# Kernel optimization log

Hardware: AMD Instinct MI355X
Metric: run time of the kernel (lower is better)

Reference implementation:

```python
import jax, jax.numpy as jnp
import numpy as np

# dims: T tokens, HID hidden, H heads, D head_dim, K conv kernel size
T, HID, H, D, K = 4096, 2048, 16, 128, 4
HD = H * D
EPS = 1e-6


def causal_conv(x, w):
    # depthwise causal conv: x [T, C], w [C, K]; y_t = sum_i w[:, i] * x_{t-K+1+i}
    xp = jnp.pad(x, ((K - 1, 0), (0, 0)))
    y = jnp.zeros_like(x)
    for i in range(K):  # small fixed kernel loop
        y = y + w[:, i] * xp[i:i + x.shape[0]]
    return y


def l2norm(x):
    return x * jax.lax.rsqrt(jnp.sum(x * x, -1, keepdims=True) + EPS)


def setup_inputs() -> dict:
    key = jax.random.key(0)
    ks = jax.random.split(key, 16)
    s = lambda n: 1.0 / np.sqrt(n)
    return {
        "hidden_states": jax.random.normal(ks[0], (T, HID), jnp.float32),
        "Wq": jax.random.normal(ks[1], (HID, HD), jnp.float32) * s(HID),
        "Wk": jax.random.normal(ks[2], (HID, HD), jnp.float32) * s(HID),
        "Wv": jax.random.normal(ks[3], (HID, HD), jnp.float32) * s(HID),
        "wq_conv": jax.random.normal(ks[4], (HD, K), jnp.float32) * s(K),
        "wk_conv": jax.random.normal(ks[5], (HD, K), jnp.float32) * s(K),
        "wv_conv": jax.random.normal(ks[6], (HD, K), jnp.float32) * s(K),
        "A_log": jax.random.uniform(ks[7], (H,), jnp.float32, 0.0, 0.5),
        "dt_bias": jax.random.normal(ks[8], (HD,), jnp.float32) * 0.1,
        "Wfa": jax.random.normal(ks[9], (HID, D), jnp.float32) * s(HID),
        "Wfb": jax.random.normal(ks[10], (D, HD), jnp.float32) * s(D),
        "Wb": jax.random.normal(ks[11], (HID, H), jnp.float32) * s(HID),
        "Wga": jax.random.normal(ks[12], (HID, D), jnp.float32) * s(HID),
        "Wgb": jax.random.normal(ks[13], (D, HD), jnp.float32) * s(D),
        "norm_w": jnp.ones((D,), jnp.float32),
        "Wo": jax.random.normal(ks[14], (HD, HID), jnp.float32) * s(HD),
    }


def reference(hidden_states, Wq, Wk, Wv, wq_conv, wk_conv, wv_conv, A_log,
              dt_bias, Wfa, Wfb, Wb, Wga, Wgb, norm_w, Wo):
    x = hidden_states
    # projections + short causal conv + SiLU
    q = jax.nn.silu(causal_conv(x @ Wq, wq_conv)).reshape(T, H, D)
    k = jax.nn.silu(causal_conv(x @ Wk, wk_conv)).reshape(T, H, D)
    v = jax.nn.silu(causal_conv(x @ Wv, wv_conv)).reshape(T, H, D)
    # fine-grained per-channel log-decay: g = -exp(A_log) * softplus(f + dt_bias), [T,H,D]
    f = (x @ Wfa) @ Wfb + dt_bias
    g = -(jnp.exp(A_log)[None, :, None]) * jax.nn.softplus(f.reshape(T, H, D))
    beta = jax.nn.sigmoid(x @ Wb)  # [T, H]
    q = l2norm(q)
    k = l2norm(k)
    scale = D ** -0.5

    def step(S, inp):  # S: [H, Dk, Dv]
        q_t, k_t, v_t, g_t, b_t = inp
        S = S * jnp.exp(g_t)[..., None]  # diagonal per-key-channel decay
        err = v_t - jnp.einsum('hkv,hk->hv', S, k_t)  # delta-rule error
        dv = b_t[:, None] * err  # beta gate
        S = S + k_t[:, :, None] * dv[:, None, :]
        o_t = jnp.einsum('hkv,hk->hv', S, q_t) * scale
        return S, o_t

    S0 = jnp.zeros((H, D, D), jnp.float32)
    _, o = jax.lax.scan(step, S0, (q, k, v, g, beta))  # o: [T, H, D]

    # gated RMSNorm then output projection
    gate = ((x @ Wga) @ Wgb).reshape(T, H, D)
    o = o * jax.lax.rsqrt(jnp.mean(o * o, -1, keepdims=True) + EPS)
    o = o * norm_w * jax.nn.silu(gate)
    return o.reshape(T, HD) @ Wo
```

## Files before the change

### kernel.cpp

```cpp
#include <hip/hip_runtime.h>
#include <hip/hip_bf16.h>
#include <math.h>

typedef __bf16 bf16_t;
typedef __bf16 bf16x8 __attribute__((ext_vector_type(8)));
typedef float  floatx4 __attribute__((ext_vector_type(4)));
typedef float  floatx2 __attribute__((ext_vector_type(2)));
typedef unsigned uintx4 __attribute__((ext_vector_type(4)));

constexpr int T_TOK = 4096;
constexpr int HID   = 2048;
constexpr int NH    = 16;
constexpr int DH    = 128;
constexpr int CH    = 2048;
constexpr int CHUNK = 16;
constexpr int NCH   = T_TOK / CHUNK;

__global__ __launch_bounds__(256) void cast_to_bf16(const float* __restrict__ in,
                                                    bf16_t* __restrict__ out, int n) {
  int i = (blockIdx.x * 256 + threadIdx.x) * 8;
  if (i >= n) return;
  float4 a = *(const float4*)(in + i);
  float4 b = *(const float4*)(in + i + 4);
  bf16x8 o;
  o[0]=(bf16_t)a.x; o[1]=(bf16_t)a.y; o[2]=(bf16_t)a.z; o[3]=(bf16_t)a.w;
  o[4]=(bf16_t)b.x; o[5]=(bf16_t)b.y; o[6]=(bf16_t)b.z; o[7]=(bf16_t)b.w;
  *(bf16x8*)(out + i) = o;
}

__global__ __launch_bounds__(256) void transpose_cast(const float* __restrict__ in,
                                                      bf16_t* __restrict__ out, int R, int C) {
  __shared__ float tile[32][33];
  int tx = threadIdx.x & 31;
  int ty = threadIdx.x >> 5;
  int r0 = blockIdx.x * 32;
  int c0 = blockIdx.y * 32;
#pragma unroll
  for (int i = 0; i < 4; i++) {
    int r = ty + i * 8;
    float v = 0.f;
    if (r0 + r < R && c0 + tx < C) v = in[(size_t)(r0 + r) * C + (c0 + tx)];
    tile[r][tx] = v;
  }
  __syncthreads();
#pragma unroll
  for (int i = 0; i < 4; i++) {
    int cr = ty + i * 8;
    if (c0 + cr < C && r0 + tx < R)
      out[(size_t)(c0 + cr) * R + (r0 + tx)] = (bf16_t)tile[tx][cr];
  }
}

template<bool OUT_BF16>
__global__ __launch_bounds__(256) void gemm_bf16(
    const bf16_t* __restrict__ A, int lda,
    const bf16_t* __restrict__ Bt, int ldb,
    void* __restrict__ Cv, int ldc, int M, int N, int K) {
  __shared__ bf16_t sA[128][40];
  __shared__ bf16_t sB[128][40];
  const int tid  = threadIdx.x;
  const int bm0  = blockIdx.x * 128;
  const int bn0  = blockIdx.y * 128;
  const int wave = tid >> 6;
  const int lane = tid & 63;
  const int wm   = (wave & 1) * 64;
  const int wn   = (wave >> 1) * 64;
  const int fm   = lane & 15;
  const int kq   = lane >> 4;

  floatx4 acc[4][4];
#pragma unroll
  for (int mi = 0; mi < 4; mi++)
#pragma unroll
    for (int ni = 0; ni < 4; ni++)
      acc[mi][ni] = (floatx4){0.f, 0.f, 0.f, 0.f};

  const int sr = tid >> 2;
  const int sk = (tid & 3) * 8;
  const bool bval0 = (bn0 + sr) < N;
  const bool bval1 = (bn0 + sr + 64) < N;
  const bf16_t* Ag0 = A + (size_t)(bm0 + sr) * lda + sk;
  const bf16_t* Ag1 = Ag0 + (size_t)64 * lda;
  const bf16_t* Bg0 = Bt + (size_t)(bn0 + sr) * ldb + sk;
  const bf16_t* Bg1 = Bg0 + (size_t)64 * ldb;

  for (int k0 = 0; k0 < K; k0 += 32) {
    float4 a0 = *(const float4*)(Ag0 + k0);
    float4 a1 = *(const float4*)(Ag1 + k0);
    float4 b0 = bval0 ? *(const float4*)(Bg0 + k0) : make_float4(0.f, 0.f, 0.f, 0.f);
    float4 b1 = bval1 ? *(const float4*)(Bg1 + k0) : make_float4(0.f, 0.f, 0.f, 0.f);
    __syncthreads();
    *(float4*)(&sA[sr][sk])      = a0;
    *(float4*)(&sA[sr + 64][sk]) = a1;
    *(float4*)(&sB[sr][sk])      = b0;
    *(float4*)(&sB[sr + 64][sk]) = b1;
    __syncthreads();
    bf16x8 afr[4], bfr[4];
#pragma unroll
    for (int i = 0; i < 4; i++) {
      afr[i] = *(const bf16x8*)(&sA[wm + i * 16 + fm][kq * 8]);
      bfr[i] = *(const bf16x8*)(&sB[wn + i * 16 + fm][kq * 8]);
    }
#pragma unroll
    for (int mi = 0; mi < 4; mi++)
#pragma unroll
      for (int ni = 0; ni < 4; ni++)
        acc[mi][ni] = __builtin_amdgcn_mfma_f32_16x16x32_bf16(afr[mi], bfr[ni], acc[mi][ni], 0, 0, 0);
  }

  const int rr = (lane >> 4) * 4;
#pragma unroll
  for (int mi = 0; mi < 4; mi++) {
#pragma unroll
    for (int r = 0; r < 4; r++) {
      const int row = bm0 + wm + mi * 16 + rr + r;
#pragma unroll
      for (int ni = 0; ni < 4; ni++) {
        const int col = bn0 + wn + ni * 16 + fm;
        if (col < N) {
          if constexpr (OUT_BF16)
            ((bf16_t*)Cv)[(size_t)row * ldc + col] = (bf16_t)acc[mi][ni][r];
          else
            ((float*)Cv)[(size_t)row * ldc + col] = acc[mi][ni][r];
        }
      }
    }
  }
}

__device__ __forceinline__ void gload_lds16(const bf16_t* g, bf16_t* l) {
  __builtin_amdgcn_global_load_lds(
      (const __attribute__((address_space(1))) void*)g,
      (__attribute__((address_space(3))) void*)l, 16, 0, 0);
}

template<bool OUT_BF16>
__global__ __launch_bounds__(256) void gemm_bf16_lds(
    const bf16_t* __restrict__ A, int lda,
    const bf16_t* __restrict__ Bt, int ldb,
    void* __restrict__ Cv, int ldc, int M, int N, int K) {
  __shared__ bf16_t sA[2][128][32];
  __shared__ bf16_t sB[2][128][32];
  const int tid  = threadIdx.x;
  const int bm0  = blockIdx.x * 128;
  const int bn0  = blockIdx.y * 128;
  const int wave = tid >> 6;
  const int lane = tid & 63;
  const int wm   = (wave & 1) * 64;
  const int wn   = (wave >> 1) * 64;
  const int fm   = lane & 15;
  const int kq   = lane >> 4;

  floatx4 acc[4][4];
#pragma unroll
  for (int mi = 0; mi < 4; mi++)
#pragma unroll
    for (int ni = 0; ni < 4; ni++)
      acc[mi][ni] = (floatx4){0.f, 0.f, 0.f, 0.f};

  const int sr = tid >> 2;
  const int sk = (tid & 3) * 8;
  const bf16_t* Ag0 = A + (size_t)(bm0 + sr) * lda + sk;
  const bf16_t* Ag1 = Ag0 + (size_t)64 * lda;
  const bf16_t* Bg0 = Bt + (size_t)(bn0 + sr) * ldb + sk;
  const bf16_t* Bg1 = Bg0 + (size_t)64 * ldb;

  auto stage = [&](int b, int k0) {
    gload_lds16(Ag0 + k0, &sA[b][16 * wave][0]);
    gload_lds16(Ag1 + k0, &sA[b][64 + 16 * wave][0]);
    gload_lds16(Bg0 + k0, &sB[b][16 * wave][0]);
    gload_lds16(Bg1 + k0, &sB[b][64 + 16 * wave][0]);
  };

  stage(0, 0);
  __syncthreads();
  int cur = 0;
  for (int k0 = 0; k0 < K; k0 += 32) {
    if (k0 + 32 < K) stage(cur ^ 1, k0 + 32);
    bf16x8 afr[4], bfr[4];
#pragma unroll
    for (int i = 0; i < 4; i++) {
      afr[i] = *(const bf16x8*)(&sA[cur][wm + i * 16 + fm][kq * 8]);
      bfr[i] = *(const bf16x8*)(&sB[cur][wn + i * 16 + fm][kq * 8]);
    }
#pragma unroll
    for (int mi = 0; mi < 4; mi++)
#pragma unroll
      for (int ni = 0; ni < 4; ni++)
        acc[mi][ni] = __builtin_amdgcn_mfma_f32_16x16x32_bf16(afr[mi], bfr[ni], acc[mi][ni], 0, 0, 0);
    __syncthreads();
    cur ^= 1;
  }

  const int rr = (lane >> 4) * 4;
#pragma unroll
  for (int mi = 0; mi < 4; mi++) {
#pragma unroll
    for (int r = 0; r < 4; r++) {
      const int row = bm0 + wm + mi * 16 + rr + r;
#pragma unroll
      for (int ni = 0; ni < 4; ni++) {
        const int col = bn0 + wn + ni * 16 + fm;
        if constexpr (OUT_BF16)
          ((bf16_t*)Cv)[(size_t)row * ldc + col] = (bf16_t)acc[mi][ni][r];
        else
          ((float*)Cv)[(size_t)row * ldc + col] = acc[mi][ni][r];
      }
    }
  }
}

template<bool L2NORM>
__global__ __launch_bounds__(256) void conv_silu(
    const bf16_t* __restrict__ raw, const float* __restrict__ wconv,
    bf16_t* __restrict__ out) {
  const int t   = blockIdx.x;
  const int tid = threadIdx.x;
  const int c0  = tid * 8;

  float w[8][4];
#pragma unroll
  for (int j = 0; j < 8; j++) {
    float4 t0 = *(const float4*)(wconv + (size_t)(c0 + j) * 4);
    w[j][0] = t0.x; w[j][1] = t0.y; w[j][2] = t0.z; w[j][3] = t0.w;
  }
  float a[8] = {};
#pragma unroll
  for (int i = 0; i < 4; i++) {
    int tr = t - 3 + i;
    if (tr < 0) continue;
    bf16x8 xr = *(const bf16x8*)(raw + (size_t)tr * CH + c0);
#pragma unroll
    for (int j = 0; j < 8; j++) a[j] += w[j][i] * (float)xr[j];
  }
  float s = 0.f;
#pragma unroll
  for (int j = 0; j < 8; j++) {
    a[j] = a[j] / (1.f + expf(-a[j]));
    s += a[j] * a[j];
  }
  float rs = 1.f;
  if constexpr (L2NORM) {
#pragma unroll
    for (int m = 1; m < 16; m <<= 1) s += __shfl_xor(s, m);
    rs = rsqrtf(s + 1e-6f);
  }
  bf16x8 r;
#pragma unroll
  for (int j = 0; j < 8; j++) r[j] = (bf16_t)(a[j] * rs);
  *(bf16x8*)(out + (size_t)t * CH + c0) = r;
}

__global__ __launch_bounds__(256) void gamma_beta(
    float* __restrict__ f_gam, const float* __restrict__ dt_bias,
    const float* __restrict__ A_log, float* __restrict__ beta_io) {
  const int t   = blockIdx.x;
  const int tid = threadIdx.x;
  const int c0  = tid * 8;
  const int h   = c0 >> 7;
  const float a_h = expf(A_log[h]);
  const size_t o0 = (size_t)t * CH + c0;
  float fv[8], db[8];
  { float4 f0 = *(const float4*)(f_gam + o0);   float4 f1 = *(const float4*)(f_gam + o0 + 4);
    fv[0]=f0.x; fv[1]=f0.y; fv[2]=f0.z; fv[3]=f0.w; fv[4]=f1.x; fv[5]=f1.y; fv[6]=f1.z; fv[7]=f1.w;
    float4 d0 = *(const float4*)(dt_bias + c0); float4 d1 = *(const float4*)(dt_bias + c0 + 4);
    db[0]=d0.x; db[1]=d0.y; db[2]=d0.z; db[3]=d0.w; db[4]=d1.x; db[5]=d1.y; db[6]=d1.z; db[7]=d1.w; }
  float og[8];
#pragma unroll
  for (int j = 0; j < 8; j++) {
    float f = fv[j] + db[j];
    float sp = (f > 20.f) ? f : log1pf(expf(f));
    og[j] = -a_h * sp;
  }
  *(float4*)(f_gam + o0)     = make_float4(og[0], og[1], og[2], og[3]);
  *(float4*)(f_gam + o0 + 4) = make_float4(og[4], og[5], og[6], og[7]);
  if (tid < NH) {
    float b = beta_io[(size_t)t * NH + tid];
    beta_io[(size_t)t * NH + tid] = 1.f / (1.f + expf(-b));
  }
}

template<int IMM>
__device__ __forceinline__ float swzf(float x) {
  return __builtin_bit_cast(float, __builtin_amdgcn_ds_swizzle(__builtin_bit_cast(int, x), IMM));
}
template<int CTRL>
__device__ __forceinline__ float dppadd(float x) {
  int v = __builtin_amdgcn_update_dpp(0, __builtin_bit_cast(int, x), CTRL, 0xF, 0xF, true);
  return x + __builtin_bit_cast(float, v);
}
__device__ __forceinline__ float cumsum16(float x) {
  x = dppadd<0x111>(x);
  x = dppadd<0x112>(x);
  x = dppadd<0x114>(x);
  x = dppadd<0x118>(x);
  return x;
}
__device__ __forceinline__ floatx2 bfpair(unsigned u) {
  floatx2 r;
  r[0] = __builtin_bit_cast(float, u << 16);
  r[1] = __builtin_bit_cast(float, u & 0xFFFF0000u);
  return r;
}

__global__ __launch_bounds__(64) void wy_prep(
    bf16_t* __restrict__ qn, bf16_t* __restrict__ kn,
    const float* __restrict__ gg, const float* __restrict__ beta,
    bf16_t* __restrict__ ktilT, float* __restrict__ Tm,
    bf16_t* __restrict__ MBf, float* __restrict__ ecT, float* __restrict__ e2T) {
  const int hc = blockIdx.x;
  const int h  = hc >> 8;
  const int c  = hc & 255;
  const int l  = threadIdx.x;
  const int tl = l & 15;
  const int gr = l >> 4;

  __shared__ bf16_t KldsT[128][24];
  __shared__ float  Wlds[16][17];
  __shared__ float  Mlds[16][17];
  __shared__ float  eclds[128], e2lds[128];
  __shared__ float  blds[16];

  const int kb0 = h * DH + gr * 8;
  const size_t rowoff = (size_t)(c * CHUNK + tl) * CH;

  if (gr == 0) blds[tl] = beta[(size_t)(c * CHUNK + tl) * NH + h];

  floatx4 wt = (floatx4){0.f, 0.f, 0.f, 0.f};
  floatx4 m  = (floatx4){0.f, 0.f, 0.f, 0.f};
  bf16x8 khs[4], qhs[4];
#pragma unroll
  for (int kb = 0; kb < 4; kb++) {
    const int ke = kb0 + kb * 32;
    float4 ga = *(const float4*)(gg + rowoff + ke);
    float4 gb = *(const float4*)(gg + rowoff + ke + 4);
    float cm[8] = {ga.x, ga.y, ga.z, ga.w, gb.x, gb.y, gb.z, gb.w};
    float lamh[8], lamt[8], ec[8], e2[8];
#pragma unroll
    for (int j = 0; j < 8; j++) {
      float cs   = cumsum16(cm[j]);
      float cmid = swzf<(7 << 5) | 0x10>(cs);
      lamh[j] = __expf(cs - cmid);
      lamt[j] = __expf(cmid - cs);
      ec[j]   = __expf(cmid);
      e2[j]   = swzf<(15 << 5) | 0x10>(lamh[j]);
    }
    if (tl == 0) {
#pragma unroll
      for (int j = 0; j < 8; j++) {
        eclds[kb * 32 + gr * 8 + j] = ec[j];
        e2lds[kb * 32 + gr * 8 + j] = e2[j];
      }
    }
    uint4 kr = *(const uint4*)(kn + rowoff + ke);
    uint4 qr = *(const uint4*)(qn + rowoff + ke);
    float kf[8], qf[8];
    { floatx2 a0 = bfpair(kr.x), a1 = bfpair(kr.y), a2 = bfpair(kr.z), a3 = bfpair(kr.w);
      kf[0]=a0[0];kf[1]=a0[1];kf[2]=a1[0];kf[3]=a1[1];kf[4]=a2[0];kf[5]=a2[1];kf[6]=a3[0];kf[7]=a3[1];
      floatx2 b0 = bfpair(qr.x), b1 = bfpair(qr.y), b2 = bfpair(qr.z), b3 = bfpair(qr.w);
      qf[0]=b0[0];qf[1]=b0[1];qf[2]=b1[0];qf[3]=b1[1];qf[4]=b2[0];qf[5]=b2[1];qf[6]=b3[0];qf[7]=b3[1]; }
    bf16x8 khat, ktil, qhat;
#pragma unroll
    for (int j = 0; j < 8; j++) {
      khat[j] = (bf16_t)(kf[j] * lamh[j]);
      ktil[j] = (bf16_t)(kf[j] * lamt[j]);
      qhat[j] = (bf16_t)(qf[j] * lamh[j]);
      khs[kb][j] = (bf16_t)(kf[j] * lamh[j] * ec[j]);
      qhs[kb][j] = (bf16_t)(qf[j] * lamh[j] * ec[j]);
    }
    wt = __builtin_amdgcn_mfma_f32_16x16x32_bf16(ktil, khat, wt, 0, 0, 0);
    m  = __builtin_amdgcn_mfma_f32_16x16x32_bf16(qhat, ktil, m,  0, 0, 0);
#pragma unroll
    for (int j = 0; j < 8; j++) KldsT[kb * 32 + gr * 8 + j][tl] = ktil[j];
  }
#pragma unroll
  for (int kb = 0; kb < 4; kb++) {
    *(uint4*)(kn + rowoff + kb0 + kb * 32) = __builtin_bit_cast(uint4, khs[kb]);
    *(uint4*)(qn + rowoff + kb0 + kb * 32) = __builtin_bit_cast(uint4, qhs[kb]);
  }
#pragma unroll
  for (int ri = 0; ri < 4; ri++) {
    Wlds[tl][4 * gr + ri] = wt[ri];
    Mlds[4 * gr + ri][tl] = (4 * gr + ri >= tl) ? m[ri] : 0.f;
  }
  {
    const int j = tl;
    float x[16];
#pragma unroll
    for (int t = 0; t < 16; t++) {
      float a = 0.f;
#pragma unroll
      for (int s = 0; s < 16; s++)
        if (s < t) a = fmaf(Wlds[t][s], x[s], a);
      x[t] = (t == j) ? 1.f : ((t > j) ? -blds[t] * a : 0.f);
    }
    if (gr == 0) {
      const float bj = blds[j];
#pragma unroll
      for (int t = 0; t < 16; t++)
        Tm[((size_t)hc * 16 + t) * 16 + j] = x[t] * bj;
    }
  }
  {
    uint4 mbo = {0, 0, 0, 0};
    if (gr < 2) {
      bf16x8 mm;
#pragma unroll
      for (int jj = 0; jj < 8; jj++) mm[jj] = (bf16_t)Mlds[tl][gr * 8 + jj];
      mbo = __builtin_bit_cast(uint4, mm);
    }
    ((uint4*)MBf)[(size_t)hc * 64 + l] = mbo;
  }
  for (int i = l; i < 128; i += 64) {
    uint4 a0 = *(const uint4*)&KldsT[i][0];
    uint4 a1 = *(const uint4*)&KldsT[i][8];
    bf16_t* dst = ktilT + ((size_t)hc * 128 + i) * 16;
    *(uint4*)dst = a0;
    *(uint4*)(dst + 8) = a1;
  }
  for (int i = l; i < 128; i += 64) {
    ecT[(size_t)hc * 128 + (i & 15) * 8 + (i >> 4)] = eclds[i];
    e2T[(size_t)hc * 128 + (i & 15) * 8 + (i >> 4)] = e2lds[i];
  }
}

__global__ __launch_bounds__(128, 1) void scan_wy3(
    const bf16_t* __restrict__ khsG, const bf16_t* __restrict__ qhsG,
    const bf16_t* __restrict__ vn, const bf16_t* __restrict__ ktilT,
    const float* __restrict__ Tm, const bf16_t* __restrict__ MBf,
    const float* __restrict__ ecT, const float* __restrict__ e2T,
    float* __restrict__ o) {
  const int h   = blockIdx.x >> 3;
  const int vt  = blockIdx.x & 7;
  const int tid = threadIdx.x;
  const int wid = tid >> 6;
  const int l   = tid & 63;
  const int tl  = l & 15;
  const int gr  = l >> 4;

  __shared__ uint4   sKQ[2][8][64];
  __shared__ floatx4 sT[2][4][64];
  __shared__ uint4   sMB[2][64];
  __shared__ uint4   sKT[2][8][64];
  __shared__ floatx4 sEC[2][4][64];
  __shared__ uint2   sV[2][64];
  __shared__ float4  sO[2][64];
  __shared__ float   SldsT[16][132];
  __shared__ float   DVlds[16][17];

  const int kb0 = h * DH + gr * 8;
  const int vb0 = h * DH + vt * 16 + gr * 4;
  const size_t hcBase = (size_t)h * NCH;
  constexpr float scale = 0.08838834764831845f;

  auto produce = [&](int c, int b) {
    const size_t rowoff = (size_t)(c * CHUNK + tl) * CH;
    const size_t hc = hcBase + c;
    uint4 kq[8];
#pragma unroll
    for (int kb = 0; kb < 4; kb++) {
      kq[kb]     = *(const uint4*)(khsG + rowoff + kb0 + kb * 32);
      kq[4 + kb] = *(const uint4*)(qhsG + rowoff + kb0 + kb * 32);
    }
    const float* Trp = Tm + (hc * 16 + tl) * 16;
    floatx4 Tv[4];
#pragma unroll
    for (int j = 0; j < 4; j++) Tv[j] = *(const floatx4*)(Trp + 4 * j);
    uint4 mbv = ((const uint4*)MBf)[hc * 64 + l];
    const int g2 = gr & 1;
    uint4 ktv[8];
#pragma unroll
    for (int kt = 0; kt < 8; kt++)
      ktv[kt] = *(const uint4*)(ktilT + (hc * 128 + kt * 16 + tl) * 16 + g2 * 8);
    floatx4 ecv[4];
    ecv[0] = *(const floatx4*)(ecT + hc * 128 + tl * 8);
    ecv[1] = *(const floatx4*)(ecT + hc * 128 + tl * 8 + 4);
    ecv[2] = *(const floatx4*)(e2T + hc * 128 + tl * 8);
    ecv[3] = *(const floatx4*)(e2T + hc * 128 + tl * 8 + 4);
    uint2 vv = *(const uint2*)(vn + rowoff + vb0);
#pragma unroll
    for (int i = 0; i < 8; i++) sKQ[b][i][l] = kq[i];
#pragma unroll
    for (int j = 0; j < 4; j++) sT[b][j][l] = Tv[j];
    sMB[b][l] = mbv;
#pragma unroll
    for (int i = 0; i < 8; i++) sKT[b][i][l] = ktv[i];
#pragma unroll
    for (int j = 0; j < 4; j++) sEC[b][j][l] = ecv[j];
    sV[b][l] = vv;
  };

  float S[8][4];
#pragma unroll
  for (int kt = 0; kt < 8; kt++)
#pragma unroll
    for (int ri = 0; ri < 4; ri++) S[kt][ri] = 0.f;

  if (wid == 1) {
    produce(0, 0);
  } else {
    for (int i = l; i < 16 * 132; i += 64) (&SldsT[0][0])[i] = 0.f;
  }
  __syncthreads();

  int cur = 0;
  for (int c = 0; c < NCH; ++c) {
    if (wid == 1) {
      if (c >= 1) {
        float4 ov = sO[cur ^ 1][l];
        const size_t rowp = (size_t)((c - 1) * CHUNK + tl) * CH;
        *(float4*)(o + rowp + vb0) = ov;
      }
      produce(c + 1 < NCH ? c + 1 : NCH - 1, cur ^ 1);
    } else {
      floatx4 p  = (floatx4){0.f, 0.f, 0.f, 0.f};
      floatx4 o1 = (floatx4){0.f, 0.f, 0.f, 0.f};
#pragma unroll
      for (int kb = 0; kb < 4; kb++) {
        float4 sa = *(const float4*)(&SldsT[tl][kb * 32 + gr * 8]);
        float4 sb = *(const float4*)(&SldsT[tl][kb * 32 + gr * 8 + 4]);
        bf16x8 s0a;
        s0a[0]=(bf16_t)sa.x; s0a[1]=(bf16_t)sa.y; s0a[2]=(bf16_t)sa.z; s0a[3]=(bf16_t)sa.w;
        s0a[4]=(bf16_t)sb.x; s0a[5]=(bf16_t)sb.y; s0a[6]=(bf16_t)sb.z; s0a[7]=(bf16_t)sb.w;
        p  = __builtin_amdgcn_mfma_f32_16x16x32_bf16(s0a, __builtin_bit_cast(bf16x8, sKQ[cur][kb][l]), p,  0, 0, 0);
        o1 = __builtin_amdgcn_mfma_f32_16x16x32_bf16(s0a, __builtin_bit_cast(bf16x8, sKQ[cur][4 + kb][l]), o1, 0, 0, 0);
      }
      float acc[4];
      { uint2 vr = sV[cur][l];
        floatx2 v01 = bfpair(vr.x), v23 = bfpair(vr.y);
        acc[0] = v01[0] - p[0]; acc[1] = v01[1] - p[1];
        acc[2] = v23[0] - p[2]; acc[3] = v23[1] - p[3]; }
      *(float4*)(&DVlds[tl][4 * gr]) = make_float4(acc[0], acc[1], acc[2], acc[3]);
      floatx4 T0 = sT[cur][0][l], T1 = sT[cur][1][l], T2 = sT[cur][2][l], T3 = sT[cur][3][l];
      float dv[4] = {0.f, 0.f, 0.f, 0.f};
#pragma unroll
      for (int s = 0; s < 16; s++) {
        const float ts = (s < 4) ? T0[s] : (s < 8) ? T1[s - 4] : (s < 12) ? T2[s - 8] : T3[s - 12];
        float4 vp = *(const float4*)(&DVlds[s][4 * gr]);
        dv[0] = fmaf(ts, vp.x, dv[0]);
        dv[1] = fmaf(ts, vp.y, dv[1]);
        dv[2] = fmaf(ts, vp.z, dv[2]);
        dv[3] = fmaf(ts, vp.w, dv[3]);
      }
#pragma unroll
      for (int ri = 0; ri < 4; ri++) DVlds[tl][4 * gr + ri] = dv[ri];
      bf16x8 dva = {};
      if (gr < 2) {
#pragma unroll
        for (int jj = 0; jj < 8; jj++) dva[jj] = (bf16_t)DVlds[gr * 8 + jj][tl];
      }
      floatx4 o2 = __builtin_amdgcn_mfma_f32_16x16x32_bf16(
          dva, __builtin_bit_cast(bf16x8, sMB[cur][l]), (floatx4){0.f, 0.f, 0.f, 0.f}, 0, 0, 0);
      sO[cur][l] = make_float4((o1[0] + o2[0]) * scale, (o1[1] + o2[1]) * scale,
                               (o1[2] + o2[2]) * scale, (o1[3] + o2[3]) * scale);
      floatx4 ec0 = sEC[cur][0][l], ec1 = sEC[cur][1][l];
      floatx4 e20 = sEC[cur][2][l], e21 = sEC[cur][3][l];
#pragma unroll
      for (int kt = 0; kt < 8; kt++) {
        const float ecK = (kt < 4) ? ec0[kt] : ec1[kt - 4];
        const float e2K = (kt < 4) ? e20[kt] : e21[kt - 4];
        floatx4 sa;
#pragma unroll
        for (int ri = 0; ri < 4; ri++) sa[ri] = ecK * S[kt][ri];
        sa = __builtin_amdgcn_mfma_f32_16x16x32_bf16(
            dva, __builtin_bit_cast(bf16x8, sKT[cur][kt][l]), sa, 0, 0, 0);
#pragma unroll
        for (int ri = 0; ri < 4; ri++) S[kt][ri] = e2K * sa[ri];
      }
#pragma unroll
      for (int kt = 0; kt < 8; kt++)
#pragma unroll
        for (int ri = 0; ri < 4; ri++)
          SldsT[4 * gr + ri][kt * 16 + tl] = S[kt][ri];
    }
    __syncthreads();
    cur ^= 1;
  }
  if (wid == 1) {
    float4 ov = sO[(NCH - 1) & 1][l];
    const size_t rowp = (size_t)((NCH - 1) * CHUNK + tl) * CH;
    *(float4*)(o + rowp + vb0) = ov;
  }
}

__global__ __launch_bounds__(256) void postprocess(
    const float* __restrict__ o, const bf16_t* __restrict__ gate,
    const float* __restrict__ norm_w, bf16_t* __restrict__ og) {
  const int t = blockIdx.x, tid = threadIdx.x;
  const int c0 = tid * 8, d0 = c0 & 127;
  const size_t o0 = (size_t)t * CH + c0;
  float ov[8], gv[8], nw[8];
  { float4 a = *(const float4*)(o + o0);    float4 b = *(const float4*)(o + o0 + 4);
    ov[0]=a.x; ov[1]=a.y; ov[2]=a.z; ov[3]=a.w; ov[4]=b.x; ov[5]=b.y; ov[6]=b.z; ov[7]=b.w;
    bf16x8 g8 = *(const bf16x8*)(gate + o0);
    for (int j = 0; j < 8; j++) gv[j] = (float)g8[j];
    float4 e = *(const float4*)(norm_w + d0); float4 f = *(const float4*)(norm_w + d0 + 4);
    nw[0]=e.x; nw[1]=e.y; nw[2]=e.z; nw[3]=e.w; nw[4]=f.x; nw[5]=f.y; nw[6]=f.z; nw[7]=f.w; }
  float ss = 0.f;
#pragma unroll
  for (int j = 0; j < 8; j++) ss += ov[j] * ov[j];
#pragma unroll
  for (int m = 1; m < 16; m <<= 1) ss += __shfl_xor(ss, m);
  const float rs = rsqrtf(ss * (1.f / 128.f) + 1e-6f);
  bf16x8 r;
#pragma unroll
  for (int j = 0; j < 8; j++) {
    float g = gv[j];
    float val = ov[j] * rs * nw[j] * (g / (1.f + expf(-g)));
    r[j] = (bf16_t)val;
  }
  *(bf16x8*)(og + o0) = r;
}

static inline void launch_gemm(const bf16_t* A, int lda, const bf16_t* Bt, int ldb,
                               void* C, int ldc, int M, int N, int K, bool obf16,
                               hipStream_t s) {
  dim3 grid(M / 128, (N + 127) / 128);
  if ((N & 127) == 0) {
    if (obf16) gemm_bf16_lds<true><<<grid, 256, 0, s>>>(A, lda, Bt, ldb, C, ldc, M, N, K);
    else       gemm_bf16_lds<false><<<grid, 256, 0, s>>>(A, lda, Bt, ldb, C, ldc, M, N, K);
  } else {
    if (obf16) gemm_bf16<true><<<grid, 256, 0, s>>>(A, lda, Bt, ldb, C, ldc, M, N, K);
    else       gemm_bf16<false><<<grid, 256, 0, s>>>(A, lda, Bt, ldb, C, ldc, M, N, K);
  }
}

extern "C" void kernel_launch(void* const* d_in, const int* in_sizes, int n_in,
                              void* d_out, int out_size, void* d_ws, size_t ws_size,
                              hipStream_t stream) {
  const float* x       = (const float*)d_in[0];
  const float* Wq      = (const float*)d_in[1];
  const float* Wk      = (const float*)d_in[2];
  const float* Wv      = (const float*)d_in[3];
  const float* wqc     = (const float*)d_in[4];
  const float* wkc     = (const float*)d_in[5];
  const float* wvc     = (const float*)d_in[6];
  const float* A_log   = (const float*)d_in[7];
  const float* dt_bias = (const float*)d_in[8];
  const float* Wfa     = (const float*)d_in[9];
  const float* Wfb     = (const float*)d_in[10];
  const float* Wb      = (const float*)d_in[11];
  const float* Wga     = (const float*)d_in[12];
  const float* Wgb     = (const float*)d_in[13];
  const float* norm_w  = (const float*)d_in[14];
  const float* Wo      = (const float*)d_in[15];

  char* w = (char*)d_ws;
  size_t off = 0;
  auto give = [&](size_t bytes) -> void* {
    size_t cur = off;
    off = (off + bytes + 255) & ~(size_t)255;
    return (void*)(w + cur);
  };
  bf16_t* Wbig = (bf16_t*)give((size_t)CH * HID * 2);
  bf16_t* WfgT = (bf16_t*)give((size_t)256 * HID * 2);
  bf16_t* WfbT = (bf16_t*)give((size_t)CH * 128 * 2);
  bf16_t* WgbT = (bf16_t*)give((size_t)CH * 128 * 2);
  bf16_t* WbT  = (bf16_t*)give((size_t)NH * HID * 2);
  bf16_t* Ax   = (bf16_t*)give((size_t)T_TOK * HID * 2);
  bf16_t* raw0 = (bf16_t*)give((size_t)T_TOK * CH * 2);
  bf16_t* qnb  = (bf16_t*)give((size_t)T_TOK * CH * 2);
  bf16_t* knb  = (bf16_t*)give((size_t)T_TOK * CH * 2);
  bf16_t* vnb  = (bf16_t*)give((size_t)T_TOK * CH * 2);
  bf16_t* f1g1 = (bf16_t*)give((size_t)T_TOK * 256 * 2);
  float*  fbuf = (float*)give((size_t)T_TOK * CH * 4);
  bf16_t* gateb= (bf16_t*)give((size_t)T_TOK * CH * 2);
  float*  betab= (float*)give((size_t)T_TOK * NH * 4);
  bf16_t* ktilT= (bf16_t*)give((size_t)NH * NCH * 128 * 16 * 2);
  float*  Tmat = (float*)give((size_t)NH * NCH * 256 * 4);
  bf16_t* MBf  = (bf16_t*)give((size_t)NH * NCH * 64 * 8 * 2);
  float*  ecTb = (float*)give((size_t)NH * NCH * 128 * 4);
  float*  e2Tb = (float*)give((size_t)NH * NCH * 128 * 4);
  float*  obuf = (float*)Ax;
  bf16_t* ogb  = qnb;

  auto tr = [&](const float* in, bf16_t* out, int R, int C) {
    transpose_cast<<<dim3((R + 31) / 32, (C + 31) / 32), 256, 0, stream>>>(in, out, R, C);
  };

  cast_to_bf16<<<dim3((T_TOK * HID) / 2048), 256, 0, stream>>>(x, Ax, T_TOK * HID);
  tr(Wfa, WfgT, HID, 128);
  tr(Wga, WfgT + (size_t)128 * HID, HID, 128);
  tr(Wfb, WfbT, 128, CH);  tr(Wgb, WgbT, 128, CH);
  tr(Wb, WbT, HID, NH);

  tr(Wq, Wbig, HID, CH);
  launch_gemm(Ax, HID, Wbig, HID, raw0, CH, T_TOK, CH, HID, true, stream);
  conv_silu<true><<<dim3(T_TOK), 256, 0, stream>>>(raw0, wqc, qnb);
  tr(Wk, Wbig, HID, CH);
  launch_gemm(Ax, HID, Wbig, HID, raw0, CH, T_TOK, CH, HID, true, stream);
  conv_silu<true><<<dim3(T_TOK), 256, 0, stream>>>(raw0, wkc, knb);
  tr(Wv, Wbig, HID, CH);
  launch_gemm(Ax, HID, Wbig, HID, raw0, CH, T_TOK, CH, HID, true, stream);
  conv_silu<false><<<dim3(T_TOK), 256, 0, stream>>>(raw0, wvc, vnb);

  launch_gemm(Ax, HID, WfgT, HID, f1g1, 256, T_TOK, 256, HID, true, stream);
  launch_gemm(Ax, HID, WbT, HID, betab, NH, T_TOK, NH, HID, false, stream);
  launch_gemm(f1g1, 256, WfbT, 128, fbuf, CH, T_TOK, CH, 128, false, stream);
  launch_gemm(f1g1 + 128, 256, WgbT, 128, gateb, CH, T_TOK, CH, 128, true, stream);
  gamma_beta<<<dim3(T_TOK), 256, 0, stream>>>(fbuf, dt_bias, A_log, betab);

  wy_prep<<<dim3(NH * NCH), 64, 0, stream>>>(qnb, knb, fbuf, betab,
                                             ktilT, Tmat, MBf, ecTb, e2Tb);
  scan_wy3<<<dim3(128), 128, 0, stream>>>(knb, qnb, vnb, ktilT, Tmat, MBf,
                                          ecTb, e2Tb, obuf);

  postprocess<<<dim3(T_TOK), 256, 0, stream>>>(obuf, gateb, norm_w, ogb);

  tr(Wo, Wbig, CH, HID);
  launch_gemm(ogb, CH, Wbig, CH, (float*)d_out, HID, T_TOK, HID, CH, false, stream);
}
```

Baseline: 958.2 us.

## Split scan producer across two wavefronts and transpose state MFMA layout

Adds a third wavefront to the chunked delta-rule scan so global-to-LDS prefetch is split between two producer waves, shortening the per-chunk producer critical path. The state update MFMA operands are swapped so S is held transposed, letting SldsT and the dv transpose use vectorized float4 LDS writes and reads instead of scalar strided ones; the decay vectors are stored untransposed and loaded per row-group. This costs more threads per block and extra LDS, and relies on the new transposed layout staying consistent across the q/k readback.

```diff
diff --git a/kernel.cpp b/kernel.cpp
--- a/kernel.cpp
+++ b/kernel.cpp
@@ -419,12 +419,12 @@
     *(uint4*)(dst + 8) = a1;
   }
   for (int i = l; i < 128; i += 64) {
-    ecT[(size_t)hc * 128 + (i & 15) * 8 + (i >> 4)] = eclds[i];
-    e2T[(size_t)hc * 128 + (i & 15) * 8 + (i >> 4)] = e2lds[i];
-  }
-}
-
-__global__ __launch_bounds__(128, 1) void scan_wy3(
+    ecT[(size_t)hc * 128 + i] = eclds[i];
+    e2T[(size_t)hc * 128 + i] = e2lds[i];
+  }
+}
+
+__global__ __launch_bounds__(192, 1) void scan_wy3(
     const bf16_t* __restrict__ khsG, const bf16_t* __restrict__ qhsG,
     const bf16_t* __restrict__ vn, const bf16_t* __restrict__ ktilT,
     const float* __restrict__ Tm, const bf16_t* __restrict__ MBf,
@@ -442,18 +442,20 @@
   __shared__ floatx4 sT[2][4][64];
   __shared__ uint4   sMB[2][64];
   __shared__ uint4   sKT[2][8][64];
-  __shared__ floatx4 sEC[2][4][64];
+  __shared__ float   sECl[2][128];
+  __shared__ float   sE2l[2][128];
   __shared__ uint2   sV[2][64];
   __shared__ float4  sO[2][64];
   __shared__ float   SldsT[16][132];
-  __shared__ float   DVlds[16][17];
+  __shared__ float   Vp[16][17];
+  __shared__ float   DVT[16][20];
 
   const int kb0 = h * DH + gr * 8;
   const int vb0 = h * DH + vt * 16 + gr * 4;
   const size_t hcBase = (size_t)h * NCH;
   constexpr float scale = 0.08838834764831845f;
 
-  auto produce = [&](int c, int b) {
+  auto produce1 = [&](int c, int b) {
     const size_t rowoff = (size_t)(c * CHUNK + tl) * CH;
     const size_t hc = hcBase + c;
     uint4 kq[8];
@@ -466,28 +468,30 @@
     floatx4 Tv[4];
 #pragma unroll
     for (int j = 0; j < 4; j++) Tv[j] = *(const floatx4*)(Trp + 4 * j);
+    uint2 vv = *(const uint2*)(vn + rowoff + vb0);
+#pragma unroll
+    for (int i = 0; i < 8; i++) sKQ[b][i][l] = kq[i];
+#pragma unroll
+    for (int j = 0; j < 4; j++) sT[b][j][l] = Tv[j];
+    sV[b][l] = vv;
+  };
+  auto produce2 = [&](int c, int b) {
+    const size_t hc = hcBase + c;
     uint4 mbv = ((const uint4*)MBf)[hc * 64 + l];
     const int g2 = gr & 1;
     uint4 ktv[8];
 #pragma unroll
     for (int kt = 0; kt < 8; kt++)
       ktv[kt] = *(const uint4*)(ktilT + (hc * 128 + kt * 16 + tl) * 16 + g2 * 8);
-    floatx4 ecv[4];
-    ecv[0] = *(const floatx4*)(ecT + hc * 128 + tl * 8);
-    ecv[1] = *(const floatx4*)(ecT + hc * 128 + tl * 8 + 4);
-    ecv[2] = *(const floatx4*)(e2T + hc * 128 + tl * 8);
-    ecv[3] = *(const floatx4*)(e2T + hc * 128 + tl * 8 + 4);
-    uint2 vv = *(const uint2*)(vn + rowoff + vb0);
-#pragma unroll
-    for (int i = 0; i < 8; i++) sKQ[b][i][l] = kq[i];
-#pragma unroll
-    for (int j = 0; j < 4; j++) sT[b][j][l] = Tv[j];
+    float ec0 = ecT[hc * 128 + l];
+    float ec1 = ecT[hc * 128 + 64 + l];
+    float e20 = e2T[hc * 128 + l];
+    float e21 = e2T[hc * 128 + 64 + l];
     sMB[b][l] = mbv;
 #pragma unroll
     for (int i = 0; i < 8; i++) sKT[b][i][l] = ktv[i];
-#pragma unroll
-    for (int j = 0; j < 4; j++) sEC[b][j][l] = ecv[j];
-    sV[b][l] = vv;
+    sECl[b][l] = ec0; sECl[b][64 + l] = ec1;
+    sE2l[b][l] = e20; sE2l[b][64 + l] = e21;
   };
 
   float S[8][4];
@@ -497,7 +501,9 @@
     for (int ri = 0; ri < 4; ri++) S[kt][ri] = 0.f;
 
   if (wid == 1) {
-    produce(0, 0);
+    produce1(0, 0);
+  } else if (wid == 2) {
+    produce2(0, 0);
   } else {
     for (int i = l; i < 16 * 132; i += 64) (&SldsT[0][0])[i] = 0.f;
   }
@@ -505,13 +511,16 @@
 
   int cur = 0;
   for (int c = 0; c < NCH; ++c) {
+    const int nxt = (c + 1 < NCH) ? c + 1 : NCH - 1;
     if (wid == 1) {
       if (c >= 1) {
         float4 ov = sO[cur ^ 1][l];
         const size_t rowp = (size_t)((c - 1) * CHUNK + tl) * CH;
         *(float4*)(o + rowp + vb0) = ov;
       }
-      produce(c + 1 < NCH ? c + 1 : NCH - 1, cur ^ 1);
+      produce1(nxt, cur ^ 1);
+    } else if (wid == 2) {
+      produce2(nxt, cur ^ 1);
     } else {
       floatx4 p  = (floatx4){0.f, 0.f, 0.f, 0.f};
       floatx4 o1 = (floatx4){0.f, 0.f, 0.f, 0.f};
@@ -530,48 +539,47 @@
         floatx2 v01 = bfpair(vr.x), v23 = bfpair(vr.y);
         acc[0] = v01[0] - p[0]; acc[1] = v01[1] - p[1];
         acc[2] = v23[0] - p[2]; acc[3] = v23[1] - p[3]; }
-      *(float4*)(&DVlds[tl][4 * gr]) = make_float4(acc[0], acc[1], acc[2], acc[3]);
+      *(float4*)(&Vp[tl][4 * gr]) = make_float4(acc[0], acc[1], acc[2], acc[3]);
       floatx4 T0 = sT[cur][0][l], T1 = sT[cur][1][l], T2 = sT[cur][2][l], T3 = sT[cur][3][l];
       float dv[4] = {0.f, 0.f, 0.f, 0.f};
 #pragma unroll
       for (int s = 0; s < 16; s++) {
         const float ts = (s < 4) ? T0[s] : (s < 8) ? T1[s - 4] : (s < 12) ? T2[s - 8] : T3[s - 12];
-        float4 vp = *(const float4*)(&DVlds[s][4 * gr]);
+        float4 vp = *(const float4*)(&Vp[s][4 * gr]);
         dv[0] = fmaf(ts, vp.x, dv[0]);
         dv[1] = fmaf(ts, vp.y, dv[1]);
         dv[2] = fmaf(ts, vp.z, dv[2]);
         dv[3] = fmaf(ts, vp.w, dv[3]);
       }
 #pragma unroll
-      for (int ri = 0; ri < 4; ri++) DVlds[tl][4 * gr + ri] = dv[ri];
+      for (int ri = 0; ri < 4; ri++) DVT[4 * gr + ri][tl] = dv[ri];
       bf16x8 dva = {};
       if (gr < 2) {
-#pragma unroll
-        for (int jj = 0; jj < 8; jj++) dva[jj] = (bf16_t)DVlds[gr * 8 + jj][tl];
+        float4 da = *(const float4*)(&DVT[tl][gr * 8]);
+        float4 db = *(const float4*)(&DVT[tl][gr * 8 + 4]);
+        dva[0]=(bf16_t)da.x; dva[1]=(bf16_t)da.y; dva[2]=(bf16_t)da.z; dva[3]=(bf16_t)da.w;
+        dva[4]=(bf16_t)db.x; dva[5]=(bf16_t)db.y; dva[6]=(bf16_t)db.z; dva[7]=(bf16_t)db.w;
       }
       floatx4 o2 = __builtin_amdgcn_mfma_f32_16x16x32_bf16(
           dva, __builtin_bit_cast(bf16x8, sMB[cur][l]), (floatx4){0.f, 0.f, 0.f, 0.f}, 0, 0, 0);
       sO[cur][l] = make_float4((o1[0] + o2[0]) * scale, (o1[1] + o2[1]) * scale,
                                (o1[2] + o2[2]) * scale, (o1[3] + o2[3]) * scale);
-      floatx4 ec0 = sEC[cur][0][l], ec1 = sEC[cur][1][l];
-      floatx4 e20 = sEC[cur][2][l], e21 = sEC[cur][3][l];
 #pragma unroll
       for (int kt = 0; kt < 8; kt++) {
-        const float ecK = (kt < 4) ? ec0[kt] : ec1[kt - 4];
-        const float e2K = (kt < 4) ? e20[kt] : e21[kt - 4];
+        floatx4 ec4 = *(const floatx4*)(&sECl[cur][16 * kt + 4 * gr]);
+        floatx4 e24 = *(const floatx4*)(&sE2l[cur][16 * kt + 4 * gr]);
         floatx4 sa;
 #pragma unroll
-        for (int ri = 0; ri < 4; ri++) sa[ri] = ecK * S[kt][ri];
+        for (int ri = 0; ri < 4; ri++) sa[ri] = ec4[ri] * S[kt][ri];
         sa = __builtin_amdgcn_mfma_f32_16x16x32_bf16(
-            dva, __builtin_bit_cast(bf16x8, sKT[cur][kt][l]), sa, 0, 0, 0);
-#pragma unroll
-        for (int ri = 0; ri < 4; ri++) S[kt][ri] = e2K * sa[ri];
+            __builtin_bit_cast(bf16x8, sKT[cur][kt][l]), dva, sa, 0, 0, 0);
+#pragma unroll
+        for (int ri = 0; ri < 4; ri++) S[kt][ri] = e24[ri] * sa[ri];
       }
 #pragma unroll
       for (int kt = 0; kt < 8; kt++)
-#pragma unroll
-        for (int ri = 0; ri < 4; ri++)
-          SldsT[4 * gr + ri][kt * 16 + tl] = S[kt][ri];
+        *(float4*)(&SldsT[tl][16 * kt + 4 * gr]) =
+            make_float4(S[kt][0], S[kt][1], S[kt][2], S[kt][3]);
     }
     __syncthreads();
     cur ^= 1;
@@ -702,7 +710,7 @@
 
   wy_prep<<<dim3(NH * NCH), 64, 0, stream>>>(qnb, knb, fbuf, betab,
                                              ktilT, Tmat, MBf, ecTb, e2Tb);
-  scan_wy3<<<dim3(128), 128, 0, stream>>>(knb, qnb, vnb, ktilT, Tmat, MBf,
+  scan_wy3<<<dim3(128), 192, 0, stream>>>(knb, qnb, vnb, ktilT, Tmat, MBf,
                                           ecTb, e2Tb, obuf);
 
   postprocess<<<dim3(T_TOK), 256, 0, stream>>>(obuf, gateb, norm_w, ogb);
```

New measurement: 1.014 ms. 1.06x slower.
